# Optimization experiments

Measured on AMD Instinct MI355X. Metric: run time of the kernel, lower is better.

Reference implementation:

```python
import jax, jax.numpy as jnp
import numpy as np

B, N_IMG, N_TXT, D, H, HD = 1, 2048, 226, 1920, 30, 64
EPS = 1e-5


def setup_inputs() -> dict:
    key = jax.random.key(0)
    ks = jax.random.split(key, 12)
    s = 0.02
    return {
        'hidden_states': jax.random.normal(ks[0], (B, N_IMG, D), jnp.float32),
        'encoder_hidden_states': jax.random.normal(ks[1], (B, N_TXT, D), jnp.float32),
        'rope_cos': jnp.cos(jax.random.uniform(ks[2], (N_IMG, HD), jnp.float32) * 6.28),
        'rope_sin': jnp.sin(jax.random.uniform(ks[3], (N_IMG, HD), jnp.float32) * 6.28),
        'Wq': s * jax.random.normal(ks[4], (D, D), jnp.float32),
        'bq': jnp.zeros((D,), jnp.float32),
        'Wk': s * jax.random.normal(ks[5], (D, D), jnp.float32),
        'bk': jnp.zeros((D,), jnp.float32),
        'Wv': s * jax.random.normal(ks[6], (D, D), jnp.float32),
        'bv': jnp.zeros((D,), jnp.float32),
        'norm_q_w': jnp.ones((HD,), jnp.float32),
        'norm_q_b': jnp.zeros((HD,), jnp.float32),
        'norm_k_w': jnp.ones((HD,), jnp.float32),
        'norm_k_b': jnp.zeros((HD,), jnp.float32),
        'Wo': s * jax.random.normal(ks[7], (D, D), jnp.float32),
        'bo': jnp.zeros((D,), jnp.float32),
    }


def _layernorm(x, w, b):
    mu = jnp.mean(x, axis=-1, keepdims=True)
    var = jnp.mean(jnp.square(x - mu), axis=-1, keepdims=True)
    return (x - mu) * jax.lax.rsqrt(var + EPS) * w + b


def _apply_rope(x, cos, sin):
    # x: [B,H,S,HD]; diffusers apply_rotary_emb with use_real, unbind_dim=-1
    xr = x.reshape(*x.shape[:-1], HD // 2, 2)
    x_real, x_imag = xr[..., 0], xr[..., 1]
    x_rot = jnp.stack([-x_imag, x_real], axis=-1).reshape(x.shape)
    return x * cos[None, None] + x_rot * sin[None, None]


def reference(hidden_states, encoder_hidden_states, rope_cos, rope_sin,
              Wq, bq, Wk, bk, Wv, bv, norm_q_w, norm_q_b, norm_k_w, norm_k_b,
              Wo, bo):
    T = encoder_hidden_states.shape[1]
    x = jnp.concatenate([encoder_hidden_states, hidden_states], axis=1)  # [B,S,D]
    S = x.shape[1]

    def proj(W, b):
        return (x @ W.T + b).reshape(B, S, H, HD).transpose(0, 2, 1, 3)  # [B,H,S,HD]

    q = _layernorm(proj(Wq, bq), norm_q_w, norm_q_b)
    k = _layernorm(proj(Wk, bk), norm_k_w, norm_k_b)
    v = proj(Wv, bv)

    # RoPE only on image tokens
    q = jnp.concatenate([q[:, :, :T], _apply_rope(q[:, :, T:], rope_cos, rope_sin)], axis=2)
    k = jnp.concatenate([k[:, :, :T], _apply_rope(k[:, :, T:], rope_cos, rope_sin)], axis=2)

    scale = 1.0 / jnp.sqrt(jnp.asarray(HD, q.dtype))
    scores = jnp.einsum('bhqd,bhkd->bhqk', q, k) * scale
    attn = jax.nn.softmax(scores, axis=-1)
    o = jnp.einsum('bhqk,bhkd->bhqd', attn, v)
    o = o.transpose(0, 2, 1, 3).reshape(B, S, H * HD)
    o = o @ Wo.T + bo

    hidden_states_out = o[:, T:]
    encoder_hidden_states_out = o[:, :T]
    return (hidden_states_out, encoder_hidden_states_out)
```

## Files before the change

### kernel.cpp

```cpp
#include <hip/hip_runtime.h>
#include <hip/hip_bf16.h>

#define S_TOT 2274
#define T_TXT 226
#define NIMG  2048
#define DM    1920
#define NH    30
#define HD    64
#define SP    2304

typedef __attribute__((ext_vector_type(8))) short bf16x8;
typedef __attribute__((ext_vector_type(4))) float f32x4;

__device__ __forceinline__ float bs2f(short u) {
  union { float f; unsigned i; } x; x.i = ((unsigned)(unsigned short)u) << 16; return x.f;
}
__device__ __forceinline__ short f2bs(float f) {
  union { __hip_bfloat16 h; short s; } u; u.h = __float2bfloat16(f); return u.s;
}
__device__ __forceinline__ __hip_bfloat16 f2b(float f) { return __float2bfloat16(f); }

__device__ __forceinline__ void gl2lds16(const void* g, void* l) {
  __builtin_amdgcn_global_load_lds((const __attribute__((address_space(1))) void*)g,
                                   (__attribute__((address_space(3))) void*)l, 16, 0, 0);
}

__device__ __forceinline__ float exp2_hw(float x) {
  float r;
  asm("v_exp_f32 %0, %1" : "=v"(r) : "v"(x));
  return r;
}

__device__ __forceinline__ int xcd_remap(int orig, int q, int r) {
  const int xcd = orig & 7, pos = orig >> 3;
  return (xcd < r ? xcd * (q + 1) : r * (q + 1) + (xcd - r) * q) + pos;
}

__global__ __launch_bounds__(256) void k_cvt(
    const float* __restrict__ hs, const float* __restrict__ enc,
    const float* __restrict__ Wq, const float* __restrict__ Wk,
    const float* __restrict__ Wv, const float* __restrict__ Wo,
    __hip_bfloat16* __restrict__ xb, __hip_bfloat16* __restrict__ Wb)
{
  const int which = blockIdx.y;
  const size_t i0 = ((size_t)blockIdx.x * 256 + threadIdx.x) * 8;
  float v[8];
  if (which == 0) {
    if (i0 >= (size_t)SP * DM) return;
    const int s = (int)(i0 / DM);
    const int c = (int)(i0 - (size_t)s * DM);
    if (s < T_TXT) {
      const float* p = enc + (size_t)s * DM + c;
#pragma unroll
      for (int e = 0; e < 8; ++e) v[e] = p[e];
    } else if (s < S_TOT) {
      const float* p = hs + (size_t)(s - T_TXT) * DM + c;
#pragma unroll
      for (int e = 0; e < 8; ++e) v[e] = p[e];
    } else {
#pragma unroll
      for (int e = 0; e < 8; ++e) v[e] = 0.0f;
    }
    bf16x8 o;
#pragma unroll
    for (int e = 0; e < 8; ++e) o[e] = f2bs(v[e]);
    *(bf16x8*)(xb + i0) = o;
  } else {
    if (i0 >= (size_t)DM * DM) return;
    const float* src = (which == 1) ? Wq : (which == 2) ? Wk : (which == 3) ? Wv : Wo;
#pragma unroll
    for (int e = 0; e < 8; ++e) v[e] = src[i0 + e];
    bf16x8 o;
#pragma unroll
    for (int e = 0; e < 8; ++e) o[e] = f2bs(v[e]);
    *(bf16x8*)(Wb + (size_t)(which - 1) * DM * DM + i0) = o;
  }
}

__global__ __launch_bounds__(256, 4) void k_qkv(
    const __hip_bfloat16* __restrict__ xb, const __hip_bfloat16* __restrict__ Wb,
    const float* __restrict__ cosb, const float* __restrict__ sinb,
    const float* __restrict__ bq, const float* __restrict__ bk,
    const float* __restrict__ bv,
    const float* __restrict__ nqw, const float* __restrict__ nqb,
    const float* __restrict__ nkw, const float* __restrict__ nkb,
    __hip_bfloat16* __restrict__ Qb, __hip_bfloat16* __restrict__ Kb,
    __hip_bfloat16* __restrict__ Vtb)
{
  __shared__ __align__(16) short As[128 * 64];
  __shared__ __align__(16) short Bs[128 * 64];
  const int t = threadIdx.x, l = t & 63, w = t >> 6;

  const int L = xcd_remap(blockIdx.x, 101, 2);
  const int bm = L % 18;
  const int yy = L / 18;
  const int mode = yy / 15;
  const int bn = yy % 15;
  const __hip_bfloat16* W = Wb + (size_t)mode * DM * DM;
  const float* bias = (mode == 0) ? bq : ((mode == 1) ? bk : bv);

  const int rt = t >> 3;
  const int lc = (t & 7) ^ (rt & 7);
  const __hip_bfloat16* aptr[4];
  const __hip_bfloat16* bptr[4];
#pragma unroll
  for (int i = 0; i < 4; ++i) {
    aptr[i] = xb + (size_t)(bm * 128 + i * 32 + rt) * DM + lc * 8;
    bptr[i] = W + (size_t)(bn * 128 + i * 32 + rt) * DM + lc * 8;
  }

  f32x4 acc[4][4];
#pragma unroll
  for (int m = 0; m < 4; ++m)
#pragma unroll
    for (int n = 0; n < 4; ++n) acc[m][n] = (f32x4){0.f, 0.f, 0.f, 0.f};

  char* AsB = (char*)As;
  char* BsB = (char*)Bs;
  const int g = l >> 4, cl = l & 15;
  const int chx = l & 7;

  for (int k0 = 0; k0 < DM; k0 += 64) {
    __syncthreads();
#pragma unroll
    for (int i = 0; i < 4; ++i) {
      gl2lds16(aptr[i], AsB + i * 4096 + w * 1024);
      gl2lds16(bptr[i], BsB + i * 4096 + w * 1024);
      aptr[i] += 64; bptr[i] += 64;
    }
    asm volatile("s_waitcnt vmcnt(0)" ::: "memory");
    __syncthreads();

    const char* Abase = AsB + ((w >> 1) * 64 + cl) * 128;
    const char* Bbase = BsB + ((w & 1) * 64 + cl) * 128;
#pragma unroll
    for (int ks = 0; ks < 2; ++ks) {
      const int choff = ((ks * 4 + g) ^ chx) * 16;
      bf16x8 af[4], bfr[4];
#pragma unroll
      for (int m = 0; m < 4; ++m) af[m]  = *(const bf16x8*)(Abase + m * 2048 + choff);
#pragma unroll
      for (int n = 0; n < 4; ++n) bfr[n] = *(const bf16x8*)(Bbase + n * 2048 + choff);
#pragma unroll
      for (int m = 0; m < 4; ++m)
#pragma unroll
        for (int n = 0; n < 4; ++n)
          acc[m][n] = __builtin_amdgcn_mfma_f32_16x16x32_bf16(af[m], bfr[n], acc[m][n], 0, 0, 0);
    }
  }

  const int n0 = bn * 128 + (w & 1) * 64;
  const int h = n0 >> 6;
  const int srow0 = bm * 128 + (w >> 1) * 64;

  if (mode < 2) {
    const float* nw = (mode == 0) ? nqw : nkw;
    const float* nb = (mode == 0) ? nqb : nkb;
    float wv[4], bvv[4], bf_[4];
#pragma unroll
    for (int n = 0; n < 4; ++n) {
      int c = n * 16 + cl;
      wv[n] = nw[c]; bvv[n] = nb[c]; bf_[n] = bias[n0 + c];
    }
    __hip_bfloat16* dst = ((mode == 0) ? Qb : Kb) + (size_t)h * SP * HD;
#pragma unroll
    for (int m = 0; m < 4; ++m) {
#pragma unroll
      for (int j = 0; j < 4; ++j) {
        int s = srow0 + m * 16 + g * 4 + j;
        float v[4];
#pragma unroll
        for (int n = 0; n < 4; ++n) v[n] = acc[m][n][j] + bf_[n];
        float s1 = v[0] + v[1] + v[2] + v[3];
        float s2 = v[0]*v[0] + v[1]*v[1] + v[2]*v[2] + v[3]*v[3];
#pragma unroll
        for (int off = 1; off < 16; off <<= 1) {
          s1 += __shfl_xor(s1, off);
          s2 += __shfl_xor(s2, off);
        }
        float mean = s1 * (1.0f / 64.0f);
        float var  = s2 * (1.0f / 64.0f) - mean * mean;
        float rstd = rsqrtf(var + 1e-5f);
        int pos = s - T_TXT; pos = pos < 0 ? 0 : (pos >= NIMG ? NIMG - 1 : pos);
        bool img = (s >= T_TXT);
#pragma unroll
        for (int n = 0; n < 4; ++n) {
          float y = (v[n] - mean) * rstd * wv[n] + bvv[n];
          float cs = cosb[pos * HD + n * 16 + cl];
          float sn = sinb[pos * HD + n * 16 + cl];
          float part = __shfl_xor(y, 1);
          float rop = (cl & 1) ? fmaf(part, sn, y * cs) : fmaf(-part, sn, y * cs);
          y = img ? rop : y;
          v[n] = (s < S_TOT) ? y : 0.0f;
        }
#pragma unroll
        for (int n = 0; n < 4; ++n)
          dst[(size_t)s * HD + n * 16 + cl] = f2b(v[n]);
      }
    }
  } else {
    float bf_[4];
#pragma unroll
    for (int n = 0; n < 4; ++n) bf_[n] = bias[n0 + n * 16 + cl];
    __hip_bfloat16* dst = Vtb + (size_t)h * HD * SP;
#pragma unroll
    for (int m = 0; m < 4; ++m) {
#pragma unroll
      for (int j = 0; j < 4; ++j) {
        int s = srow0 + m * 16 + g * 4 + j;
#pragma unroll
        for (int n = 0; n < 4; ++n) {
          float y = acc[m][n][j] + bf_[n];
          y = (s < S_TOT) ? y : 0.0f;
          dst[(size_t)(n * 16 + cl) * SP + s] = f2b(y);
        }
      }
    }
  }
}

__global__ __launch_bounds__(256) void k_attn(
    const __hip_bfloat16* __restrict__ Qb, const __hip_bfloat16* __restrict__ Kb,
    const __hip_bfloat16* __restrict__ Vtb, __hip_bfloat16* __restrict__ Ob)
{
  __shared__ __align__(16) short Ks[2][64 * 64];
  __shared__ __align__(16) short Vs[2][64 * 64];
  __shared__ __align__(16) short Pl[4][16 * 64];
  const int t = threadIdx.x, l = t & 63, w = t >> 6;
  const int g = l >> 4, cl = l & 15;
  const int cb = cl & 7;

  const int L = xcd_remap(blockIdx.x, 67, 4);
  const int h = L / 18;
  const int bm = L % 18;
  const int q0 = bm * 128 + w * 32;

  const __hip_bfloat16* Qh = Qb + (size_t)h * SP * HD;
  const __hip_bfloat16* Kh = Kb + (size_t)h * SP * HD;
  const __hip_bfloat16* Vh = Vtb + (size_t)h * HD * SP;
  char* myP = (char*)&Pl[w][0];
  char* KsB = (char*)Ks;
  char* VsB = (char*)Vs;

  const int srow = l >> 3;
  const int slot = l & 7;

#pragma unroll
  for (int i = 0; i < 2; ++i) {
    const int seg = w * 2 + i;
    const int row = seg * 8 + srow;
    const int ch = slot ^ (row & 7);
    gl2lds16(Kh + (size_t)row * HD + ch * 8, KsB + seg * 1024);
    gl2lds16(Vh + (size_t)row * SP + 0 + ch * 8, VsB + seg * 1024);
  }

  const float QS = 0.125f * 1.4426950408889634f;
  bf16x8 qf[2][2];
#pragma unroll
  for (int m = 0; m < 2; ++m)
#pragma unroll
    for (int ks = 0; ks < 2; ++ks) {
      int qr = q0 + m * 16 + cl;
      bf16x8 raw = *(const bf16x8*)(Qh + (size_t)qr * HD + ks * 32 + g * 8);
      bf16x8 s8;
#pragma unroll
      for (int e = 0; e < 8; ++e) s8[e] = f2bs(bs2f(raw[e]) * QS);
      qf[m][ks] = s8;
    }

  const bf16x8 ones8 = {0x3F80, 0x3F80, 0x3F80, 0x3F80, 0x3F80, 0x3F80, 0x3F80, 0x3F80};

  f32x4 o[2][4], smv[2];
#pragma unroll
  for (int m = 0; m < 2; ++m) {
    smv[m] = (f32x4){0.f, 0.f, 0.f, 0.f};
#pragma unroll
    for (int n = 0; n < 4; ++n) o[m][n] = (f32x4){0.f, 0.f, 0.f, 0.f};
  }

  const int NT = SP / 64;
  for (int tt = 0; tt < NT; ++tt) {
    const int kv = tt * 64;
    const int cur = tt & 1;

    if (tt + 1 < NT) {
      const int kvn = kv + 64;
#pragma unroll
      for (int i = 0; i < 2; ++i) {
        const int seg = w * 2 + i;
        const int row = seg * 8 + srow;
        const int ch = slot ^ (row & 7);
        gl2lds16(Kh + (size_t)(kvn + row) * HD + ch * 8, KsB + (cur ^ 1) * 8192 + seg * 1024);
        gl2lds16(Vh + (size_t)row * SP + kvn + ch * 8, VsB + (cur ^ 1) * 8192 + seg * 1024);
      }
      asm volatile("s_waitcnt vmcnt(4)" ::: "memory");
    } else {
      asm volatile("s_waitcnt vmcnt(0)" ::: "memory");
    }
    __syncthreads();

    const char* Kbuf = KsB + cur * 8192;
    const char* Vbuf = VsB + cur * 8192;

    f32x4 sc[2][4];
    __builtin_amdgcn_s_setprio(1);
#pragma unroll
    for (int n = 0; n < 4; ++n) {
      bf16x8 kf0 = *(const bf16x8*)(Kbuf + (n * 16 + cl) * 128 + (((0 + g) ^ cb) << 4));
      bf16x8 kf1 = *(const bf16x8*)(Kbuf + (n * 16 + cl) * 128 + (((4 + g) ^ cb) << 4));
#pragma unroll
      for (int m = 0; m < 2; ++m) {
        f32x4 a = (f32x4){0.f, 0.f, 0.f, 0.f};
        a = __builtin_amdgcn_mfma_f32_16x16x32_bf16(qf[m][0], kf0, a, 0, 0, 0);
        a = __builtin_amdgcn_mfma_f32_16x16x32_bf16(qf[m][1], kf1, a, 0, 0, 0);
        sc[m][n] = a;
      }
    }
    __builtin_amdgcn_s_setprio(0);

    bf16x8 vf[4][2];
#pragma unroll
    for (int n = 0; n < 4; ++n) {
      vf[n][0] = *(const bf16x8*)(Vbuf + (n * 16 + cl) * 128 + (((0 + g) ^ cb) << 4));
      vf[n][1] = *(const bf16x8*)(Vbuf + (n * 16 + cl) * 128 + (((4 + g) ^ cb) << 4));
    }

    if (tt == NT - 1) {
#pragma unroll
      for (int n = 0; n < 4; ++n) {
        if (kv + n * 16 + cl >= S_TOT) {
#pragma unroll
          for (int m = 0; m < 2; ++m)
#pragma unroll
            for (int r = 0; r < 4; ++r) sc[m][n][r] = -1e30f;
        }
      }
    }

#pragma unroll
    for (int m = 0; m < 2; ++m) {
#pragma unroll
      for (int n = 0; n < 4; ++n)
#pragma unroll
        for (int r = 0; r < 4; ++r) {
          float p = exp2_hw(sc[m][n][r]);
          int row = g * 4 + r;
          int chunk = ((n * 16 + cl) >> 3) ^ (row & 7);
          *(short*)(myP + row * 128 + chunk * 16 + 2 * (cl & 7)) = f2bs(p);
        }
      bf16x8 pa[2];
#pragma unroll
      for (int ks = 0; ks < 2; ++ks)
        pa[ks] = *(const bf16x8*)(myP + cl * 128 + (((ks * 4 + g) ^ cb) << 4));
      __builtin_amdgcn_s_setprio(1);
#pragma unroll
      for (int n = 0; n < 4; ++n) {
        o[m][n] = __builtin_amdgcn_mfma_f32_16x16x32_bf16(pa[0], vf[n][0], o[m][n], 0, 0, 0);
        o[m][n] = __builtin_amdgcn_mfma_f32_16x16x32_bf16(pa[1], vf[n][1], o[m][n], 0, 0, 0);
      }
      smv[m] = __builtin_amdgcn_mfma_f32_16x16x32_bf16(pa[0], ones8, smv[m], 0, 0, 0);
      smv[m] = __builtin_amdgcn_mfma_f32_16x16x32_bf16(pa[1], ones8, smv[m], 0, 0, 0);
      __builtin_amdgcn_s_setprio(0);
    }

    __syncthreads();
  }

#pragma unroll
  for (int m = 0; m < 2; ++m)
#pragma unroll
    for (int r = 0; r < 4; ++r) {
      float inv = 1.0f / smv[m][r];
      int s = q0 + m * 16 + g * 4 + r;
#pragma unroll
      for (int n = 0; n < 4; ++n) {
        float y = (s < S_TOT) ? o[m][n][r] * inv : 0.0f;
        Ob[(size_t)s * DM + h * HD + n * 16 + cl] = f2b(y);
      }
    }
}

__global__ __launch_bounds__(256, 4) void k_out(
    const __hip_bfloat16* __restrict__ Ob, const __hip_bfloat16* __restrict__ Wo,
    const float* __restrict__ bo, float* __restrict__ out)
{
  __shared__ __align__(16) short As[64 * 64];
  __shared__ __align__(16) short Bs[128 * 64];
  const int t = threadIdx.x, l = t & 63, w = t >> 6;

  const int L = xcd_remap(blockIdx.x, 67, 4);
  const int bm = L % 36;
  const int bn = L / 36;

  const int rt = t >> 3;
  const int lc = (t & 7) ^ (rt & 7);
  const __hip_bfloat16* aptr[2];
  const __hip_bfloat16* bptr[4];
#pragma unroll
  for (int i = 0; i < 2; ++i)
    aptr[i] = Ob + (size_t)(bm * 64 + i * 32 + rt) * DM + lc * 8;
#pragma unroll
  for (int i = 0; i < 4; ++i)
    bptr[i] = Wo + (size_t)(bn * 128 + i * 32 + rt) * DM + lc * 8;

  f32x4 acc[2][4];
#pragma unroll
  for (int m = 0; m < 2; ++m)
#pragma unroll
    for (int n = 0; n < 4; ++n) acc[m][n] = (f32x4){0.f, 0.f, 0.f, 0.f};

  char* AsB = (char*)As;
  char* BsB = (char*)Bs;
  const int g = l >> 4, cl = l & 15;
  const int chx = l & 7;

  for (int k0 = 0; k0 < DM; k0 += 64) {
    __syncthreads();
#pragma unroll
    for (int i = 0; i < 2; ++i) {
      gl2lds16(aptr[i], AsB + i * 4096 + w * 1024);
      aptr[i] += 64;
    }
#pragma unroll
    for (int i = 0; i < 4; ++i) {
      gl2lds16(bptr[i], BsB + i * 4096 + w * 1024);
      bptr[i] += 64;
    }
    asm volatile("s_waitcnt vmcnt(0)" ::: "memory");
    __syncthreads();

    const char* Abase = AsB + ((w >> 1) * 32 + cl) * 128;
    const char* Bbase = BsB + ((w & 1) * 64 + cl) * 128;
#pragma unroll
    for (int ks = 0; ks < 2; ++ks) {
      const int choff = ((ks * 4 + g) ^ chx) * 16;
      bf16x8 af[2], bfr[4];
#pragma unroll
      for (int m = 0; m < 2; ++m) af[m]  = *(const bf16x8*)(Abase + m * 2048 + choff);
#pragma unroll
      for (int n = 0; n < 4; ++n) bfr[n] = *(const bf16x8*)(Bbase + n * 2048 + choff);
#pragma unroll
      for (int m = 0; m < 2; ++m)
#pragma unroll
        for (int n = 0; n < 4; ++n)
          acc[m][n] = __builtin_amdgcn_mfma_f32_16x16x32_bf16(af[m], bfr[n], acc[m][n], 0, 0, 0);
    }
  }

  const int n0 = bn * 128 + (w & 1) * 64;
  const int srow0 = bm * 64 + (w >> 1) * 32;
  float bf_[4];
#pragma unroll
  for (int n = 0; n < 4; ++n) bf_[n] = bo[n0 + n * 16 + cl];

#pragma unroll
  for (int m = 0; m < 2; ++m) {
#pragma unroll
    for (int j = 0; j < 4; ++j) {
      int s = srow0 + m * 16 + g * 4 + j;
      if (s < S_TOT) {
        size_t rowoff = (s >= T_TXT) ? (size_t)(s - T_TXT) * DM
                                     : (size_t)NIMG * DM + (size_t)s * DM;
#pragma unroll
        for (int n = 0; n < 4; ++n)
          out[rowoff + n0 + n * 16 + cl] = acc[m][n][j] + bf_[n];
      }
    }
  }
}

extern "C" void kernel_launch(void* const* d_in, const int* in_sizes, int n_in,
                              void* d_out, int out_size, void* d_ws, size_t ws_size,
                              hipStream_t stream) {
  const float* hs   = (const float*)d_in[0];
  const float* enc  = (const float*)d_in[1];
  const float* cosb = (const float*)d_in[2];
  const float* sinb = (const float*)d_in[3];
  const float* Wq   = (const float*)d_in[4];
  const float* bq   = (const float*)d_in[5];
  const float* Wk   = (const float*)d_in[6];
  const float* bk   = (const float*)d_in[7];
  const float* Wv   = (const float*)d_in[8];
  const float* bv   = (const float*)d_in[9];
  const float* nqw  = (const float*)d_in[10];
  const float* nqb  = (const float*)d_in[11];
  const float* nkw  = (const float*)d_in[12];
  const float* nkb  = (const float*)d_in[13];
  const float* Wo   = (const float*)d_in[14];
  const float* bo   = (const float*)d_in[15];
  float* out = (float*)d_out;

  const size_t NE = (size_t)NH * SP * HD;
  __hip_bfloat16* Qb  = (__hip_bfloat16*)d_ws;
  __hip_bfloat16* Kb  = Qb + NE;
  __hip_bfloat16* Vtb = Kb + NE;
  __hip_bfloat16* Ob  = Vtb + NE;
  __hip_bfloat16* xb  = Ob + NE;
  __hip_bfloat16* Wb  = xb + (size_t)SP * DM;

  k_cvt<<<dim3(2160, 5), 256, 0, stream>>>(hs, enc, Wq, Wk, Wv, Wo, xb, Wb);
  k_qkv<<<dim3(810), 256, 0, stream>>>(xb, Wb, cosb, sinb, bq, bk, bv,
                                       nqw, nqb, nkw, nkb, Qb, Kb, Vtb);
  k_attn<<<dim3(540), 256, 0, stream>>>(Qb, Kb, Vtb, Ob);
  k_out<<<dim3(540), 256, 0, stream>>>(Ob, Wb + 3 * (size_t)DM * DM, bo, out);
}
```

Before: 233.5 us.

## Split attention KV range in two and add a combine kernel

Each attention block now handles half of the key/value tiles, which doubles the grid from 540 to 1080 blocks. Each block writes unnormalized bf16 partial outputs and per-row softmax sums, and a new k_comb kernel adds the two partials and divides by the summed denominators. The aim is to fill the CUs better and cut the tail of a grid that is only about two waves deep. The cost is an extra launch, a round trip of the partials through memory, and rounding the unnormalized partials to bf16. The partial buffers reuse the dead x and Wq/Wk/Wv workspace regions.

Measured after the change: 215.3 us. -7.8%, faster.

```diff
diff --git a/kernel.cpp b/kernel.cpp
--- a/kernel.cpp
+++ b/kernel.cpp
@@ -221,7 +221,8 @@
 
 __global__ __launch_bounds__(256) void k_attn(
     const __hip_bfloat16* __restrict__ Qb, const __hip_bfloat16* __restrict__ Kb,
-    const __hip_bfloat16* __restrict__ Vtb, __hip_bfloat16* __restrict__ Ob)
+    const __hip_bfloat16* __restrict__ Vtb,
+    __hip_bfloat16* __restrict__ pO, float* __restrict__ sums)
 {
   __shared__ __align__(16) short Ks[2][64 * 64];
   __shared__ __align__(16) short Vs[2][64 * 64];
@@ -230,10 +231,15 @@
   const int g = l >> 4, cl = l & 15;
   const int cb = cl & 7;
 
-  const int L = xcd_remap(blockIdx.x, 67, 4);
-  const int h = L / 18;
-  const int bm = L % 18;
+  const int L = xcd_remap(blockIdx.x, 135, 0);
+  const int h = L / 36;
+  const int rem = L % 36;
+  const int split = rem / 18;
+  const int bm = rem % 18;
   const int q0 = bm * 128 + w * 32;
+
+  const int NT = SP / 64;
+  const int T0 = split * 18, T1 = T0 + 18;
 
   const __hip_bfloat16* Qh = Qb + (size_t)h * SP * HD;
   const __hip_bfloat16* Kh = Kb + (size_t)h * SP * HD;
@@ -250,8 +256,8 @@
     const int seg = w * 2 + i;
     const int row = seg * 8 + srow;
     const int ch = slot ^ (row & 7);
-    gl2lds16(Kh + (size_t)row * HD + ch * 8, KsB + seg * 1024);
-    gl2lds16(Vh + (size_t)row * SP + 0 + ch * 8, VsB + seg * 1024);
+    gl2lds16(Kh + (size_t)(T0 * 64 + row) * HD + ch * 8, KsB + seg * 1024);
+    gl2lds16(Vh + (size_t)row * SP + T0 * 64 + ch * 8, VsB + seg * 1024);
   }
 
   const float QS = 0.125f * 1.4426950408889634f;
@@ -278,12 +284,11 @@
     for (int n = 0; n < 4; ++n) o[m][n] = (f32x4){0.f, 0.f, 0.f, 0.f};
   }
 
-  const int NT = SP / 64;
-  for (int tt = 0; tt < NT; ++tt) {
+  for (int tt = T0; tt < T1; ++tt) {
     const int kv = tt * 64;
     const int cur = tt & 1;
 
-    if (tt + 1 < NT) {
+    if (tt + 1 < T1) {
       const int kvn = kv + 64;
 #pragma unroll
       for (int i = 0; i < 2; ++i) {
@@ -366,18 +371,37 @@
     __syncthreads();
   }
 
+  __hip_bfloat16* myPO = pO + (size_t)split * SP * DM;
+  float* mySums = sums + (size_t)split * NH * SP + (size_t)h * SP;
 #pragma unroll
   for (int m = 0; m < 2; ++m)
 #pragma unroll
     for (int r = 0; r < 4; ++r) {
-      float inv = 1.0f / smv[m][r];
       int s = q0 + m * 16 + g * 4 + r;
-#pragma unroll
-      for (int n = 0; n < 4; ++n) {
-        float y = (s < S_TOT) ? o[m][n][r] * inv : 0.0f;
-        Ob[(size_t)s * DM + h * HD + n * 16 + cl] = f2b(y);
-      }
-    }
+      if (cl == 0) mySums[s] = smv[m][r];
+#pragma unroll
+      for (int n = 0; n < 4; ++n)
+        myPO[(size_t)s * DM + h * HD + n * 16 + cl] = f2b(o[m][n][r]);
+    }
+}
+
+__global__ __launch_bounds__(256) void k_comb(
+    const __hip_bfloat16* __restrict__ pO, const float* __restrict__ sums,
+    __hip_bfloat16* __restrict__ Ob)
+{
+  const size_t i0 = ((size_t)blockIdx.x * 256 + threadIdx.x) * 8;
+  const int s = (int)(i0 / DM);
+  const int c = (int)(i0 - (size_t)s * DM);
+  const int h = c >> 6;
+  bf16x8 a = *(const bf16x8*)(pO + i0);
+  bf16x8 b = *(const bf16x8*)(pO + (size_t)SP * DM + i0);
+  const float s0 = sums[(size_t)h * SP + s];
+  const float s1 = sums[(size_t)NH * SP + (size_t)h * SP + s];
+  const float inv = 1.0f / (s0 + s1);
+  bf16x8 o;
+#pragma unroll
+  for (int e = 0; e < 8; ++e) o[e] = f2bs((bs2f(a[e]) + bs2f(b[e])) * inv);
+  *(bf16x8*)(Ob + i0) = o;
 }
 
 __global__ __launch_bounds__(256, 4) void k_out(
@@ -497,10 +521,13 @@
   __hip_bfloat16* Ob  = Vtb + NE;
   __hip_bfloat16* xb  = Ob + NE;
   __hip_bfloat16* Wb  = xb + (size_t)SP * DM;
+  __hip_bfloat16* pO   = xb;
+  float*          sums = (float*)(Wb + 2 * (size_t)DM * DM);
 
   k_cvt<<<dim3(2160, 5), 256, 0, stream>>>(hs, enc, Wq, Wk, Wv, Wo, xb, Wb);
   k_qkv<<<dim3(810), 256, 0, stream>>>(xb, Wb, cosb, sinb, bq, bk, bv,
                                        nqw, nqb, nkw, nkb, Qb, Kb, Vtb);
-  k_attn<<<dim3(540), 256, 0, stream>>>(Qb, Kb, Vtb, Ob);
+  k_attn<<<dim3(1080), 256, 0, stream>>>(Qb, Kb, Vtb, pO, sums);
+  k_comb<<<dim3(2160), 256, 0, stream>>>(pO, sums, Ob);
   k_out<<<dim3(540), 256, 0, stream>>>(Ob, Wb + 3 * (size_t)DM * DM, bo, out);
 }
```
